# Optimization experiments

Hardware: AMD Instinct MI355X
Metric: run time of the kernel (lower is better)

The kernel has to match this reference:

```python
import jax, jax.numpy as jnp
import numpy as np

D_MODEL = 768
D_HEAD = 64
BATCH = 2
SEQ = 4096


def setup_inputs() -> dict:
    key = jax.random.key(0)
    k1, k2, k3, k4, k5 = jax.random.split(key, 5)
    x = jax.random.normal(k1, (BATCH, SEQ, D_MODEL), dtype=jnp.float32)
    # causal mask as the module expects: (seq_len, seq_len) float, 1 where attend allowed
    mask = jnp.tril(jnp.ones((SEQ, SEQ), dtype=jnp.float32))
    # weights initialized like the module: randn / sqrt(d_model)
    scale = 1.0 / np.sqrt(D_MODEL)
    Wq = jax.random.normal(k2, (D_HEAD, D_MODEL), dtype=jnp.float32) * scale
    Wk = jax.random.normal(k3, (D_HEAD, D_MODEL), dtype=jnp.float32) * scale
    Wv = jax.random.normal(k4, (D_HEAD, D_MODEL), dtype=jnp.float32) * scale
    Wo = jax.random.normal(k5, (D_MODEL, D_HEAD), dtype=jnp.float32) * scale
    return {"x": x, "mask": mask, "Wq": Wq, "Wk": Wk, "Wv": Wv, "Wo": Wo}


def reference(x, mask, Wq, Wk, Wv, Wo):
    # q,k,v: (B, S, d_head); Linear with weight (out,in) => x @ W.T
    q = jnp.einsum('bsm,hm->bsh', x, Wq)
    k = jnp.einsum('bsm,hm->bsh', x, Wk)
    v = jnp.einsum('bsm,hm->bsh', x, Wv)
    scores = jnp.einsum('bqd,bkd->bqk', q, k) / np.sqrt(D_HEAD)  # (B,S,S)
    seq_len = x.shape[1]
    m = mask[:seq_len, :seq_len]
    # faithful to the torch code: tril(scores) - 1e10 * (1 - mask)
    scores = jnp.tril(scores) - 1e10 * (1.0 - m)
    attn = jax.nn.softmax(scores, axis=-1)
    z = jnp.einsum('bqk,bkd->bqd', attn, v)  # (B,S,d_head)
    out = jnp.einsum('bsh,mh->bsm', z, Wo)   # (B,S,d_model)
    return out
```

## Files before the change

### kernel.cpp

```cpp
#include <hip/hip_runtime.h>
#include <stdint.h>

#define SEQ 4096
#define DM 768
#define DH 64

typedef __attribute__((ext_vector_type(8))) short short8;
typedef __attribute__((ext_vector_type(4))) short short4v;
typedef __attribute__((ext_vector_type(4))) float f32x4;
typedef __attribute__((ext_vector_type(2))) uint32_t uint2v;

#define LOG2E 1.4426950408889634f

static __device__ __forceinline__ short bf16r(float f) {
  union { float f; uint32_t u; } v; v.f = f;
  uint32_t u = v.u;
  return (short)((u + 0x7FFFu + ((u >> 16) & 1u)) >> 16);
}

static __device__ __forceinline__ float bf16f(uint16_t u) {
  union { uint32_t u; float f; } v; v.u = ((uint32_t)u) << 16;
  return v.f;
}

static __device__ __forceinline__ uint32_t cvtpk(float a, float b) {
  uint32_t r;
  asm("v_cvt_pk_bf16_f32 %0, %1, %2" : "=v"(r) : "v"(a), "v"(b));
  return r;
}

static __device__ __forceinline__ int swz(int row, int b) {
  return row * 128 + (b ^ ((row & 7) << 4));
}

__global__ __launch_bounds__(256) void convert_w(
    const float* __restrict__ Wq, const float* __restrict__ Wk,
    const float* __restrict__ Wv, const float* __restrict__ Wo,
    uint16_t* __restrict__ Wb, uint16_t* __restrict__ Wob) {
  int id = blockIdx.x * 256 + threadIdx.x;
  if (id < 36864) {
    int row = id / 192, c4 = id % 192;
    const float* src = (row < 64) ? (Wq + (size_t)row * DM)
                     : (row < 128) ? (Wk + (size_t)(row - 64) * DM)
                                   : (Wv + (size_t)(row - 128) * DM);
    const float sc = (row < 64) ? (0.125f * LOG2E) : 1.0f;
    float4 v = *(const float4*)(src + c4 * 4);
    short4v pk = { bf16r(v.x * sc), bf16r(v.y * sc), bf16r(v.z * sc), bf16r(v.w * sc) };
    *(short4v*)(Wb + (size_t)row * DM + c4 * 4) = pk;
  } else {
    int t = id - 36864;
    int row = t >> 4, c4 = t & 15;
    float4 v = *(const float4*)(Wo + (size_t)row * DH + c4 * 4);
    short4v pk = { bf16r(v.x), bf16r(v.y), bf16r(v.z), bf16r(v.w) };
    *(short4v*)(Wob + (size_t)row * DH + c4 * 4) = pk;
  }
}

__global__ __launch_bounds__(256) void qkv_proj(
    const float* __restrict__ x, const uint16_t* __restrict__ Wb,
    uint16_t* __restrict__ qg, uint16_t* __restrict__ kg, uint16_t* __restrict__ vg) {
  __shared__ char smem[4096 + 12288] __attribute__((aligned(16)));
  char* Xl = smem;
  char* Wl = smem + 4096;
  const int tid = threadIdx.x;
  const int lane = tid & 63, wv = tid >> 6;
  const int l15 = lane & 15, l4 = lane >> 4;
  const int row0 = blockIdx.x * 32;
  const int nh = blockIdx.y;
  const uint16_t* wbh = Wb + (size_t)nh * 96 * DM;

  const int xr = tid >> 4, xc4 = tid & 15;
  const int wr0 = tid >> 3, wb16 = tid & 7;
  const int mh = wv & 1, ng = wv >> 1;

  f32x4 acc[3];
  #pragma unroll
  for (int j = 0; j < 3; ++j) acc[j] = (f32x4){0.f, 0.f, 0.f, 0.f};

  float4 xreg[2];
  short8 wreg[3];
  xreg[0] = *(const float4*)(x + (size_t)(row0 + xr) * DM + xc4 * 4);
  xreg[1] = *(const float4*)(x + (size_t)(row0 + 16 + xr) * DM + xc4 * 4);
  #pragma unroll
  for (int i = 0; i < 3; ++i)
    wreg[i] = *(const short8*)(wbh + (size_t)(wr0 + i * 32) * DM + wb16 * 8);

  for (int t = 0; t < 12; ++t) {
    __syncthreads();
    {
      uint2v p0 = { cvtpk(xreg[0].x, xreg[0].y), cvtpk(xreg[0].z, xreg[0].w) };
      *(uint2v*)(Xl + swz(xr, xc4 * 8)) = p0;
      uint2v p1 = { cvtpk(xreg[1].x, xreg[1].y), cvtpk(xreg[1].z, xreg[1].w) };
      *(uint2v*)(Xl + swz(xr + 16, xc4 * 8)) = p1;
    }
    #pragma unroll
    for (int i = 0; i < 3; ++i)
      *(short8*)(Wl + swz(wr0 + i * 32, wb16 * 16)) = wreg[i];
    __syncthreads();
    if (t < 11) {
      const int k0n = (t + 1) * 64;
      xreg[0] = *(const float4*)(x + (size_t)(row0 + xr) * DM + k0n + xc4 * 4);
      xreg[1] = *(const float4*)(x + (size_t)(row0 + 16 + xr) * DM + k0n + xc4 * 4);
      #pragma unroll
      for (int i = 0; i < 3; ++i)
        wreg[i] = *(const short8*)(wbh + (size_t)(wr0 + i * 32) * DM + k0n + wb16 * 8);
    }
    #pragma unroll
    for (int kc = 0; kc < 2; ++kc) {
      short8 af = *(const short8*)(Xl + swz(mh * 16 + l15, kc * 64 + l4 * 16));
      #pragma unroll
      for (int j = 0; j < 3; ++j) {
        int tl = ng * 3 + j;
        short8 bfv = *(const short8*)(Wl + swz(tl * 16 + l15, kc * 64 + l4 * 16));
        acc[j] = __builtin_amdgcn_mfma_f32_16x16x32_bf16(af, bfv, acc[j], 0, 0, 0);
      }
    }
  }
  #pragma unroll
  for (int j = 0; j < 3; ++j) {
    int NT = nh * 6 + ng * 3 + j;
    uint16_t* dst = (NT < 4) ? qg : (NT < 8) ? kg : vg;
    int cb = (NT & 3) * 16 + l15;
    #pragma unroll
    for (int r = 0; r < 4; ++r) {
      int row = row0 + mh * 16 + l4 * 4 + r;
      dst[(size_t)row * DH + cb] = (uint16_t)bf16r(acc[j][r]);
    }
  }
}

__global__ __launch_bounds__(256) void attn_split(
    const uint16_t* __restrict__ qg, const uint16_t* __restrict__ kg,
    const uint16_t* __restrict__ vg, uint16_t* __restrict__ zg,
    uint16_t* __restrict__ Opart, float* __restrict__ Ml, int CHUNK, int MAXCH) {
  __shared__ char smem[32768 + 4 * 2048] __attribute__((aligned(16)));

  const int tid = threadIdx.x;
  const int lane = tid & 63, wv = tid >> 6;
  const int l15 = lane & 15, l4 = lane >> 4;
  const int qt = blockIdx.x, ch = blockIdx.y, b = blockIdx.z;
  const int q0 = qt << 6;
  const int kv_lim = q0 + 64;
  const int kv_begin = ch * CHUNK;
  if (kv_begin >= kv_lim) return;
  const int kv_end = min(kv_begin + CHUNK, kv_lim);
  const int ntiles = (kv_end - kv_begin) >> 6;

  const uint16_t* qb = qg + (size_t)b * SEQ * DH;
  const uint16_t* kb = kg + (size_t)b * SEQ * DH;
  const uint16_t* vb = vg + (size_t)b * SEQ * DH;

  const int qrow = q0 + wv * 16 + l15;
  short8 qf0 = *(const short8*)(qb + (size_t)qrow * DH + l4 * 8);
  short8 qf1 = *(const short8*)(qb + (size_t)qrow * DH + 32 + l4 * 8);

  int koffA[4], koffB[4], voffA[4], voffB[4];
  #pragma unroll
  for (int n = 0; n < 4; ++n) {
    koffA[n] = swz(n * 16 + l15, l4 * 16);
    koffB[n] = swz(n * 16 + l15, 64 + l4 * 16);
    int dr = n * 16 + l15;
    voffA[n] = 8192 + dr * 128 + ((l4 * 16) ^ ((dr & 7) << 4));
    voffB[n] = 8192 + dr * 128 + ((64 + l4 * 16) ^ ((dr & 7) << 4));
  }
  int pwoff[4];
  #pragma unroll
  for (int n = 0; n < 4; ++n) pwoff[n] = 32768 + wv * 2048 + swz(l15, n * 32 + l4 * 8);
  const int proff0 = 32768 + wv * 2048 + swz(l15, l4 * 16);
  const int proff1 = 32768 + wv * 2048 + swz(l15, 64 + l4 * 16);

  const int ku = tid - 128;
  const int vg_ = tid >> 3, vdg = tid & 7;
  short8 sreg[4];
  int soff[8];
  if (tid >= 128) {
    #pragma unroll
    for (int i = 0; i < 4; ++i) {
      int c = ku + (i << 7);
      soff[i] = swz(c >> 3, (c & 7) * 16);
    }
  } else {
    #pragma unroll
    for (int j = 0; j < 8; ++j) {
      int d = vdg * 8 + j;
      soff[j] = 8192 + d * 128 + ((vg_ * 8) ^ ((d & 7) << 4));
    }
  }

#define LOAD_REGS(KV0)                                                              \
  if (tid >= 128) {                                                                 \
    _Pragma("unroll")                                                               \
    for (int i = 0; i < 4; ++i) {                                                   \
      int c = ku + (i << 7);                                                        \
      sreg[i] = *(const short8*)(kb + (size_t)((KV0) + (c >> 3)) * DH + (c & 7) * 8); \
    }                                                                               \
  } else {                                                                          \
    _Pragma("unroll")                                                               \
    for (int i = 0; i < 4; ++i)                                                     \
      sreg[i] = *(const short8*)(vb + (size_t)((KV0) + vg_ * 4 + i) * DH + vdg * 8); \
  }

#define STAGE_WRITE(BUF)                                                            \
  {                                                                                 \
    char* base_ = smem + ((BUF) << 14);                                             \
    if (tid >= 128) {                                                               \
      _Pragma("unroll")                                                             \
      for (int i = 0; i < 4; ++i) *(short8*)(base_ + soff[i]) = sreg[i];            \
    } else {                                                                        \
      _Pragma("unroll")                                                             \
      for (int j = 0; j < 8; ++j) {                                                 \
        short4v pk = { sreg[0][j], sreg[1][j], sreg[2][j], sreg[3][j] };            \
        *(short4v*)(base_ + soff[j]) = pk;                                          \
      }                                                                             \
    }                                                                               \
  }

  LOAD_REGS(kv_begin);
  STAGE_WRITE(0);

  f32x4 oaccT[4];
  #pragma unroll
  for (int n = 0; n < 4; ++n) oaccT[n] = (f32x4){0.f, 0.f, 0.f, 0.f};
  float lrun = 0.f;

  for (int T = 0; T < ntiles; ++T) {
    const int kv0 = kv_begin + (T << 6);
    const bool more = (T + 1 < ntiles);
    if (more) { LOAD_REGS(kv0 + 64); }
    __syncthreads();
    char* cb_ = smem + ((T & 1) << 14);

    f32x4 sacc[4];
    #pragma unroll
    for (int n = 0; n < 4; ++n) sacc[n] = (f32x4){0.f, 0.f, 0.f, 0.f};
    __builtin_amdgcn_s_setprio(1);
    #pragma unroll
    for (int n = 0; n < 4; ++n) {
      short8 kf0 = *(const short8*)(cb_ + koffA[n]);
      sacc[n] = __builtin_amdgcn_mfma_f32_16x16x32_bf16(kf0, qf0, sacc[n], 0, 0, 0);
      short8 kf1 = *(const short8*)(cb_ + koffB[n]);
      sacc[n] = __builtin_amdgcn_mfma_f32_16x16x32_bf16(kf1, qf1, sacc[n], 0, 0, 0);
    }
    __builtin_amdgcn_s_setprio(0);

    if (more) { STAGE_WRITE((T + 1) & 1); }

    if (kv0 + 63 > q0) {
      #pragma unroll
      for (int n = 0; n < 4; ++n) {
        #pragma unroll
        for (int r = 0; r < 4; ++r) {
          int kvg = kv0 + n * 16 + l4 * 4 + r;
          if (kvg > qrow) sacc[n][r] = -1e30f;
        }
      }
    }

    float ls = 0.f;
    #pragma unroll
    for (int n = 0; n < 4; ++n) {
      #pragma unroll
      for (int r = 0; r < 4; ++r) {
        float p = __builtin_amdgcn_exp2f(sacc[n][r]);
        sacc[n][r] = p;
        ls += p;
      }
    }
    ls += __shfl_xor(ls, 16);
    ls += __shfl_xor(ls, 32);
    lrun += ls;

    #pragma unroll
    for (int n = 0; n < 4; ++n) {
      uint2v pk = { cvtpk(sacc[n][0], sacc[n][1]), cvtpk(sacc[n][2], sacc[n][3]) };
      *(uint2v*)(smem + pwoff[n]) = pk;
    }
    asm volatile("s_waitcnt lgkmcnt(0)" ::: "memory");
    short8 pa0 = *(const short8*)(smem + proff0);
    short8 pa1 = *(const short8*)(smem + proff1);
    __builtin_amdgcn_s_setprio(1);
    #pragma unroll
    for (int n = 0; n < 4; ++n) {
      short8 vf0 = *(const short8*)(cb_ + voffA[n]);
      oaccT[n] = __builtin_amdgcn_mfma_f32_16x16x32_bf16(vf0, pa0, oaccT[n], 0, 0, 0);
      short8 vf1 = *(const short8*)(cb_ + voffB[n]);
      oaccT[n] = __builtin_amdgcn_mfma_f32_16x16x32_bf16(vf1, pa1, oaccT[n], 0, 0, 0);
    }
    __builtin_amdgcn_s_setprio(0);
  }
#undef LOAD_REGS
#undef STAGE_WRITE

  const int rl = wv * 16 + l15;
  if (MAXCH == 1) {
    float invl = 1.0f / lrun;
    uint16_t* zb = zg + (size_t)b * SEQ * DH;
    #pragma unroll
    for (int n = 0; n < 4; ++n) {
      short4v pk = { bf16r(oaccT[n][0] * invl), bf16r(oaccT[n][1] * invl),
                     bf16r(oaccT[n][2] * invl), bf16r(oaccT[n][3] * invl) };
      *(short4v*)(zb + (size_t)(q0 + rl) * DH + n * 16 + l4 * 4) = pk;
    }
  } else {
    const size_t slot = ((size_t)(b << 6) + qt) * MAXCH + ch;
    uint16_t* op = Opart + slot * 4096;
    #pragma unroll
    for (int n = 0; n < 4; ++n) {
      short4v pk = { bf16r(oaccT[n][0]), bf16r(oaccT[n][1]),
                     bf16r(oaccT[n][2]), bf16r(oaccT[n][3]) };
      *(short4v*)(op + (size_t)rl * 64 + n * 16 + l4 * 4) = pk;
    }
    if (l4 == 0) Ml[slot * 64 + rl] = lrun;
  }
}

__global__ __launch_bounds__(256) void out_proj(
    const uint16_t* __restrict__ Opart, const float* __restrict__ Ml,
    const uint16_t* __restrict__ zg, const uint16_t* __restrict__ Wob,
    float* __restrict__ out, int CHUNK, int MAXCH) {
  __shared__ char smem[4096 + 32768] __attribute__((aligned(16)));
  char* Zl = smem;
  char* Wl = smem + 4096;
  const int tid = threadIdx.x;
  const int lane = tid & 63, wv = tid >> 6;
  const int l15 = lane & 15, l4 = lane >> 4;
  const int row0 = blockIdx.x * 32;
  const int col0 = blockIdx.y * 256;

  {
    const int r = tid >> 3, c0 = (tid & 7) << 3;
    if (MAXCH == 1) {
      short8 v = *(const short8*)(zg + (size_t)(row0 + r) * DH + c0);
      *(short8*)(Zl + swz(r, c0 * 2)) = v;
    } else {
      const int b = row0 >> 12;
      const int rlb = row0 & 4095;
      const int qt = rlb >> 6, q0 = qt << 6;
      const int row_local = (rlb & 63) + r;
      const int nch = (q0 + 64 + CHUNK - 1) / CHUNK;
      const size_t sbase = ((size_t)(b << 6) + qt) * MAXCH;
      float a[8] = {0.f, 0.f, 0.f, 0.f, 0.f, 0.f, 0.f, 0.f};
      float wsum = 0.f;
      for (int ch = 0; ch < nch; ++ch) {
        const size_t s = sbase + ch;
        wsum += Ml[s * 64 + row_local];
        short8 v = *(const short8*)(Opart + s * 4096 + (size_t)row_local * 64 + c0);
        #pragma unroll
        for (int j = 0; j < 8; ++j) a[j] += bf16f((uint16_t)v[j]);
      }
      float inv = 1.0f / wsum;
      short8 pk;
      #pragma unroll
      for (int j = 0; j < 8; ++j) pk[j] = bf16r(a[j] * inv);
      *(short8*)(Zl + swz(r, c0 * 2)) = pk;
    }
  }
  #pragma unroll
  for (int i = 0; i < 8; ++i) {
    int id = tid + (i << 8);
    int m = id >> 3, c8 = id & 7;
    short8 vw = *(const short8*)(Wob + (size_t)(col0 + m) * DH + c8 * 8);
    *(short8*)(Wl + swz(m, c8 * 16)) = vw;
  }
  __syncthreads();

  const int mh = wv & 1, ng = wv >> 1;
  short8 af0 = *(const short8*)(Zl + swz(mh * 16 + l15, l4 * 16));
  short8 af1 = *(const short8*)(Zl + swz(mh * 16 + l15, 64 + l4 * 16));
  f32x4 acc[8];
  #pragma unroll
  for (int j = 0; j < 8; ++j) acc[j] = (f32x4){0.f, 0.f, 0.f, 0.f};
  #pragma unroll
  for (int j = 0; j < 8; ++j) {
    int nt = ng * 8 + j;
    short8 b0 = *(const short8*)(Wl + swz(nt * 16 + l15, l4 * 16));
    acc[j] = __builtin_amdgcn_mfma_f32_16x16x32_bf16(af0, b0, acc[j], 0, 0, 0);
    short8 b1 = *(const short8*)(Wl + swz(nt * 16 + l15, 64 + l4 * 16));
    acc[j] = __builtin_amdgcn_mfma_f32_16x16x32_bf16(af1, b1, acc[j], 0, 0, 0);
  }
  #pragma unroll
  for (int j = 0; j < 8; ++j) {
    int nt = ng * 8 + j;
    #pragma unroll
    for (int r = 0; r < 4; ++r) {
      int row = row0 + mh * 16 + l4 * 4 + r;
      int col = col0 + nt * 16 + l15;
      out[(size_t)row * DM + col] = acc[j][r];
    }
  }
}

extern "C" void kernel_launch(void* const* d_in, const int* in_sizes, int n_in,
                              void* d_out, int out_size, void* d_ws, size_t ws_size,
                              hipStream_t stream) {
  const float* x  = (const float*)d_in[0];
  const float* Wq = (const float*)d_in[2];
  const float* Wk = (const float*)d_in[3];
  const float* Wv = (const float*)d_in[4];
  const float* Wo = (const float*)d_in[5];
  float* out = (float*)d_out;

  const size_t N = (size_t)2 * SEQ * DH;
  uint16_t* qg = (uint16_t*)d_ws;
  uint16_t* kg = qg + N;
  uint16_t* vg = kg + N;
  uint16_t* zg = vg + N;
  uint16_t* Wb = zg + N;
  const size_t WBE = (size_t)192 * DM;
  uint16_t* Wob = Wb + WBE;
  const size_t WOE = (size_t)DM * DH;
  uint16_t* Opart = Wob + WOE;

  int maxch = 16;
  while (maxch > 1) {
    size_t slots = (size_t)2 * 64 * maxch;
    size_t need = 4 * N * 2 + WBE * 2 + WOE * 2 + slots * (4096 * 2 + 64 * 4);
    if (need <= ws_size) break;
    maxch >>= 1;
  }
  const int CHUNK = SEQ / maxch;
  float* Ml = (float*)(Opart + (size_t)2 * 64 * maxch * 4096);

  convert_w<<<192, 256, 0, stream>>>(Wq, Wk, Wv, Wo, Wb, Wob);
  qkv_proj<<<dim3(256, 2), 256, 0, stream>>>(x, Wb, qg, kg, vg);
  attn_split<<<dim3(64, maxch, 2), 256, 0, stream>>>(qg, kg, vg, zg, Opart, Ml,
                                                     CHUNK, maxch);
  out_proj<<<dim3(256, 3), 256, 0, stream>>>(Opart, Ml, zg, Wob, out, CHUNK, maxch);
}
```

Before: 49.79 us.

## Pre-swizzle QKV weights and double-buffer qkv_proj with direct global-to-LDS loads

convert_w now writes the bf16 QKV weights in a tile-major, pre-swizzled layout that matches the LDS tile image. qkv_proj can then copy weight tiles straight into shared memory with global_load_lds, skipping the register round trip. The LDS tiles for x and W are double-buffered, which removes one barrier per k-step and lets the next tile's loads overlap the MFMAs. In exchange, LDS use goes up to 32KB per block and correctness depends on the async LDS writes being complete when the barrier is reached.

```diff
diff --git a/kernel.cpp b/kernel.cpp
--- a/kernel.cpp
+++ b/kernel.cpp
@@ -33,23 +33,38 @@
   return row * 128 + (b ^ ((row & 7) << 4));
 }
 
+static __device__ __forceinline__ void glds16(const void* g, void* l) {
+  __builtin_amdgcn_global_load_lds(
+      (const __attribute__((address_space(1))) uint32_t*)g,
+      (__attribute__((address_space(3))) uint32_t*)l, 16, 0, 0);
+}
+
 __global__ __launch_bounds__(256) void convert_w(
     const float* __restrict__ Wq, const float* __restrict__ Wk,
     const float* __restrict__ Wv, const float* __restrict__ Wo,
-    uint16_t* __restrict__ Wb, uint16_t* __restrict__ Wob) {
+    uint16_t* __restrict__ Wbp, uint16_t* __restrict__ Wob) {
   int id = blockIdx.x * 256 + threadIdx.x;
-  if (id < 36864) {
-    int row = id / 192, c4 = id % 192;
+  if (id < 18432) {
+    int nh = id / 9216, rem = id % 9216;
+    int t = rem / 768, rem2 = rem % 768;
+    int r = rem2 >> 3, g = rem2 & 7;
+    int row = nh * 96 + r;
     const float* src = (row < 64) ? (Wq + (size_t)row * DM)
                      : (row < 128) ? (Wk + (size_t)(row - 64) * DM)
                                    : (Wv + (size_t)(row - 128) * DM);
     const float sc = (row < 64) ? (0.125f * LOG2E) : 1.0f;
-    float4 v = *(const float4*)(src + c4 * 4);
-    short4v pk = { bf16r(v.x * sc), bf16r(v.y * sc), bf16r(v.z * sc), bf16r(v.w * sc) };
-    *(short4v*)(Wb + (size_t)row * DM + c4 * 4) = pk;
-  } else {
-    int t = id - 36864;
-    int row = t >> 4, c4 = t & 15;
+    float4 v0 = *(const float4*)(src + t * 64 + g * 8);
+    float4 v1 = *(const float4*)(src + t * 64 + g * 8 + 4);
+    union { uint32_t u[4]; short8 s; } pk;
+    pk.u[0] = cvtpk(v0.x * sc, v0.y * sc);
+    pk.u[1] = cvtpk(v0.z * sc, v0.w * sc);
+    pk.u[2] = cvtpk(v1.x * sc, v1.y * sc);
+    pk.u[3] = cvtpk(v1.z * sc, v1.w * sc);
+    char* dst = (char*)Wbp + (size_t)nh * 147456 + t * 12288 + swz(r, g * 16);
+    *(short8*)dst = pk.s;
+  } else if (id < 30720) {
+    int tt = id - 18432;
+    int row = tt >> 4, c4 = tt & 15;
     float4 v = *(const float4*)(Wo + (size_t)row * DH + c4 * 4);
     short4v pk = { bf16r(v.x), bf16r(v.y), bf16r(v.z), bf16r(v.w) };
     *(short4v*)(Wob + (size_t)row * DH + c4 * 4) = pk;
@@ -57,20 +72,17 @@
 }
 
 __global__ __launch_bounds__(256) void qkv_proj(
-    const float* __restrict__ x, const uint16_t* __restrict__ Wb,
+    const float* __restrict__ x, const uint16_t* __restrict__ Wbp,
     uint16_t* __restrict__ qg, uint16_t* __restrict__ kg, uint16_t* __restrict__ vg) {
-  __shared__ char smem[4096 + 12288] __attribute__((aligned(16)));
-  char* Xl = smem;
-  char* Wl = smem + 4096;
+  __shared__ char smem[32768] __attribute__((aligned(16)));
   const int tid = threadIdx.x;
   const int lane = tid & 63, wv = tid >> 6;
   const int l15 = lane & 15, l4 = lane >> 4;
   const int row0 = blockIdx.x * 32;
   const int nh = blockIdx.y;
-  const uint16_t* wbh = Wb + (size_t)nh * 96 * DM;
+  const char* wsrc = (const char*)Wbp + (size_t)nh * 147456;
 
   const int xr = tid >> 4, xc4 = tid & 15;
-  const int wr0 = tid >> 3, wb16 = tid & 7;
   const int mh = wv & 1, ng = wv >> 1;
 
   f32x4 acc[3];
@@ -78,42 +90,51 @@
   for (int j = 0; j < 3; ++j) acc[j] = (f32x4){0.f, 0.f, 0.f, 0.f};
 
   float4 xreg[2];
-  short8 wreg[3];
+  #pragma unroll
+  for (int i = 0; i < 3; ++i)
+    glds16(wsrc + wv * 3072 + i * 1024 + lane * 16,
+           smem + 8192 + wv * 3072 + i * 1024);
   xreg[0] = *(const float4*)(x + (size_t)(row0 + xr) * DM + xc4 * 4);
   xreg[1] = *(const float4*)(x + (size_t)(row0 + 16 + xr) * DM + xc4 * 4);
-  #pragma unroll
-  for (int i = 0; i < 3; ++i)
-    wreg[i] = *(const short8*)(wbh + (size_t)(wr0 + i * 32) * DM + wb16 * 8);
+  {
+    uint2v p0 = { cvtpk(xreg[0].x, xreg[0].y), cvtpk(xreg[0].z, xreg[0].w) };
+    *(uint2v*)(smem + swz(xr, xc4 * 8)) = p0;
+    uint2v p1 = { cvtpk(xreg[1].x, xreg[1].y), cvtpk(xreg[1].z, xreg[1].w) };
+    *(uint2v*)(smem + swz(xr + 16, xc4 * 8)) = p1;
+  }
 
   for (int t = 0; t < 12; ++t) {
     __syncthreads();
-    {
-      uint2v p0 = { cvtpk(xreg[0].x, xreg[0].y), cvtpk(xreg[0].z, xreg[0].w) };
-      *(uint2v*)(Xl + swz(xr, xc4 * 8)) = p0;
-      uint2v p1 = { cvtpk(xreg[1].x, xreg[1].y), cvtpk(xreg[1].z, xreg[1].w) };
-      *(uint2v*)(Xl + swz(xr + 16, xc4 * 8)) = p1;
-    }
-    #pragma unroll
-    for (int i = 0; i < 3; ++i)
-      *(short8*)(Wl + swz(wr0 + i * 32, wb16 * 16)) = wreg[i];
-    __syncthreads();
+    const int buf = t & 1;
     if (t < 11) {
+      #pragma unroll
+      for (int i = 0; i < 3; ++i)
+        glds16(wsrc + (t + 1) * 12288 + wv * 3072 + i * 1024 + lane * 16,
+               smem + 8192 + (buf ^ 1) * 12288 + wv * 3072 + i * 1024);
       const int k0n = (t + 1) * 64;
       xreg[0] = *(const float4*)(x + (size_t)(row0 + xr) * DM + k0n + xc4 * 4);
       xreg[1] = *(const float4*)(x + (size_t)(row0 + 16 + xr) * DM + k0n + xc4 * 4);
+    }
+    {
+      char* Xl = smem + buf * 4096;
+      char* Wl = smem + 8192 + buf * 12288;
       #pragma unroll
-      for (int i = 0; i < 3; ++i)
-        wreg[i] = *(const short8*)(wbh + (size_t)(wr0 + i * 32) * DM + k0n + wb16 * 8);
-    }
-    #pragma unroll
-    for (int kc = 0; kc < 2; ++kc) {
-      short8 af = *(const short8*)(Xl + swz(mh * 16 + l15, kc * 64 + l4 * 16));
-      #pragma unroll
-      for (int j = 0; j < 3; ++j) {
-        int tl = ng * 3 + j;
-        short8 bfv = *(const short8*)(Wl + swz(tl * 16 + l15, kc * 64 + l4 * 16));
-        acc[j] = __builtin_amdgcn_mfma_f32_16x16x32_bf16(af, bfv, acc[j], 0, 0, 0);
+      for (int kc = 0; kc < 2; ++kc) {
+        short8 af = *(const short8*)(Xl + swz(mh * 16 + l15, kc * 64 + l4 * 16));
+        #pragma unroll
+        for (int j = 0; j < 3; ++j) {
+          int tl = ng * 3 + j;
+          short8 bfv = *(const short8*)(Wl + swz(tl * 16 + l15, kc * 64 + l4 * 16));
+          acc[j] = __builtin_amdgcn_mfma_f32_16x16x32_bf16(af, bfv, acc[j], 0, 0, 0);
+        }
       }
+    }
+    if (t < 11) {
+      char* Xn = smem + (buf ^ 1) * 4096;
+      uint2v p0 = { cvtpk(xreg[0].x, xreg[0].y), cvtpk(xreg[0].z, xreg[0].w) };
+      *(uint2v*)(Xn + swz(xr, xc4 * 8)) = p0;
+      uint2v p1 = { cvtpk(xreg[1].x, xreg[1].y), cvtpk(xreg[1].z, xreg[1].w) };
+      *(uint2v*)(Xn + swz(xr + 16, xc4 * 8)) = p1;
     }
   }
   #pragma unroll
@@ -405,9 +426,9 @@
   uint16_t* kg = qg + N;
   uint16_t* vg = kg + N;
   uint16_t* zg = vg + N;
-  uint16_t* Wb = zg + N;
+  uint16_t* Wbp = zg + N;
   const size_t WBE = (size_t)192 * DM;
-  uint16_t* Wob = Wb + WBE;
+  uint16_t* Wob = Wbp + WBE;
   const size_t WOE = (size_t)DM * DH;
   uint16_t* Opart = Wob + WOE;
 
@@ -421,8 +442,8 @@
   const int CHUNK = SEQ / maxch;
   float* Ml = (float*)(Opart + (size_t)2 * 64 * maxch * 4096);
 
-  convert_w<<<192, 256, 0, stream>>>(Wq, Wk, Wv, Wo, Wb, Wob);
-  qkv_proj<<<dim3(256, 2), 256, 0, stream>>>(x, Wb, qg, kg, vg);
+  convert_w<<<120, 256, 0, stream>>>(Wq, Wk, Wv, Wo, Wbp, Wob);
+  qkv_proj<<<dim3(256, 2), 256, 0, stream>>>(x, Wbp, qg, kg, vg);
   attn_split<<<dim3(64, maxch, 2), 256, 0, stream>>>(qg, kg, vg, zg, Opart, Ml,
                                                      CHUNK, maxch);
   out_proj<<<dim3(256, 3), 256, 0, stream>>>(Opart, Ml, zg, Wob, out, CHUNK, maxch);
```

After: 48.91 us. About the same (-1.8%).
